# Performance work log

Hardware: AMD Instinct MI355X
Metric: run time of the kernel (lower is better)

The kernel has to match this reference:

```python
import jax, jax.numpy as jnp
import numpy as np

B, S, D = 32, 8192, 128
SPARSITY = 0.5
CLUSTER = 4
HID = 256
MEM = 128
NCLS = 10
MASK_KEY = jax.random.key(1234)


def setup_inputs() -> dict:
    key = jax.random.key(0)
    ks = jax.random.split(key, 8)
    cin = CLUSTER * D  # 512
    return {
        "x": jax.random.normal(ks[0], (B, S, D), dtype=jnp.float32),
        "memory": jax.random.normal(ks[1], (B, MEM), dtype=jnp.float32),
        "W_fc": jax.random.normal(ks[2], (HID, cin), dtype=jnp.float32) / np.sqrt(cin),
        "b_fc": jax.random.normal(ks[3], (HID,), dtype=jnp.float32) * 0.01,
        "W_mem": jax.random.normal(ks[4], (MEM, HID), dtype=jnp.float32) / np.sqrt(HID),
        "b_mem": jax.random.normal(ks[5], (MEM,), dtype=jnp.float32) * 0.01,
        "W_out": jax.random.normal(ks[6], (NCLS, MEM), dtype=jnp.float32) / np.sqrt(MEM),
        "b_out": jax.random.normal(ks[7], (NCLS,), dtype=jnp.float32) * 0.01,
    }


def reference(x, memory, W_fc, b_fc, W_mem, b_mem, W_out, b_out):
    # --- SparseInformationExtraction: top-k tokens by L2 norm ---
    k = int(SPARSITY * S)  # 4096
    token_norms = jnp.linalg.norm(x, axis=-1)          # (B, S)
    _, topk_idx = jax.lax.top_k(token_norms, k)        # (B, k), sorted desc like torch.topk
    sparse_x = jnp.take_along_axis(x, topk_idx[:, :, None], axis=1)  # (B, k, D)

    # --- HierarchicalClustering: group CLUSTER tokens ---
    num_clusters = k // CLUSTER                        # 1024
    clustered = sparse_x.reshape(B, num_clusters, CLUSTER * D)  # (B, 1024, 512)

    # --- DynamicMaskingActivation: linear + bernoulli mask + relu ---
    h = jnp.einsum('bnc,hc->bnh', clustered, W_fc) + b_fc       # (B, 1024, HID)
    mask = jax.random.bernoulli(MASK_KEY, p=SPARSITY, shape=h.shape).astype(h.dtype)
    h = jax.nn.relu(h * mask)

    # --- SparseMemory: mean-pool + linear + residual relu ---
    x_compressed = jnp.mean(h, axis=1)                           # (B, HID)
    updated_memory = jax.nn.relu(x_compressed @ W_mem.T + b_mem + memory)  # (B, MEM)

    # --- output head ---
    output = updated_memory @ W_out.T + b_out                    # (B, NCLS)
    return (output, updated_memory)
```

## Files before the change

kernel.cpp:

```cpp
#include <hip/hip_runtime.h>
#include <stdint.h>

#define NB 32
#define NS 8192
#define ND 128
#define KTOP 4096
#define NCLUST 1024
#define CIN 512
#define HIDN 256
#define NMEM 128
#define NCLS 10
#define HALFCNT 4194304u

typedef unsigned long long ull;
typedef __attribute__((ext_vector_type(8))) short bf16x8;
typedef __attribute__((ext_vector_type(4))) float f32x4;

__device__ __forceinline__ unsigned int rotl32(unsigned int v, int r) {
  return (v << r) | (v >> (32 - r));
}

__device__ __forceinline__ void threefry_block(unsigned int& x0, unsigned int& x1) {
  const unsigned int k0 = 0u;
  const unsigned int k1 = 1234u;
  const unsigned int k2 = 0x1BD11BDAu ^ 0u ^ 1234u;
  x0 += k0; x1 += k1;
#define TF_R(r) { x0 += x1; x1 = rotl32(x1, (r)); x1 ^= x0; }
  TF_R(13) TF_R(15) TF_R(26) TF_R(6)   x0 += k1; x1 += k2 + 1u;
  TF_R(17) TF_R(29) TF_R(16) TF_R(24)  x0 += k2; x1 += k0 + 2u;
  TF_R(13) TF_R(15) TF_R(26) TF_R(6)   x0 += k0; x1 += k1 + 3u;
  TF_R(17) TF_R(29) TF_R(16) TF_R(24)  x0 += k1; x1 += k2 + 4u;
  TF_R(13) TF_R(15) TF_R(26) TF_R(6)   x0 += k2; x1 += k0 + 5u;
#undef TF_R
}

__device__ __forceinline__ unsigned int f2bf(float f) {
  unsigned int u = __float_as_uint(f);
  return (u + 0x7fffu + ((u >> 16) & 1u)) >> 16;
}
__device__ __forceinline__ unsigned int pack2bf(float lo, float hi) {
  return f2bf(lo) | (f2bf(hi) << 16);
}

__device__ __forceinline__ void gload_lds16(const void* g, void* l) {
  __builtin_amdgcn_global_load_lds(
      (const __attribute__((address_space(1))) unsigned int*)g,
      (__attribute__((address_space(3))) unsigned int*)l, 16, 0, 0);
}

__device__ __forceinline__ ull shfl_xor_u64(ull x, int m) {
  unsigned int lo = (unsigned int)x, hi = (unsigned int)(x >> 32);
  lo = (unsigned int)__shfl_xor((int)lo, m);
  hi = (unsigned int)__shfl_xor((int)hi, m);
  return ((ull)hi << 32) | lo;
}

#define NORM_BLOCKS 32768
__global__ __launch_bounds__(256) void norms_kernel(
    const float* __restrict__ x, ull* __restrict__ keys,
    float* __restrict__ xc, const float* __restrict__ Wfc,
    unsigned short* __restrict__ Wbf) {
  const int blk = blockIdx.x;
  if (blk >= NORM_BLOCKS) {
    const int t = (blk - NORM_BLOCKS) * 256 + threadIdx.x;
    const float4* s = (const float4*)(Wfc + (size_t)t * 8);
    const float4 a = s[0], b = s[1];
    uint4 o;
    o.x = pack2bf(a.x, a.y); o.y = pack2bf(a.z, a.w);
    o.z = pack2bf(b.x, b.y); o.w = pack2bf(b.z, b.w);
    *(uint4*)(Wbf + (size_t)t * 8) = o;
    return;
  }
  const int t = blk * 256 + threadIdx.x;
  if (t < NB * HIDN) xc[t] = 0.0f;
  const int token = t >> 5;
  const int l = t & 31;
  const float4 v = ((const float4*)(x + (size_t)token * ND))[l];
  float ss = v.x * v.x + v.y * v.y + v.z * v.z + v.w * v.w;
#pragma unroll
  for (int off = 16; off >= 1; off >>= 1) ss += __shfl_xor(ss, off);
  if (l == 0) {
    const float nrm = sqrtf(ss);
    const unsigned int ub = ~__float_as_uint(nrm);
    keys[token] = ((ull)ub << 32) | (unsigned int)(token & (NS - 1));
  }
}

#define CMPEX(J, K, HF)                                                 \
  {                                                                     \
    _Pragma("unroll") for (int r = 0; r < 8; ++r) {                     \
      if ((r & (J)) == 0) {                                             \
        const int i0 = (tid << 3) + r;                                  \
        const bool up2 = (((i0 & (K)) == 0) != (HF));                   \
        const ull lo = v[r], hi = v[r | (J)];                           \
        const ull mn = lo < hi ? lo : hi;                               \
        const ull mx = lo < hi ? hi : lo;                               \
        v[r] = up2 ? mn : mx;                                           \
        v[r | (J)] = up2 ? mx : mn;                                     \
      }                                                                 \
    }                                                                   \
  }

__global__ __launch_bounds__(512) void sortA_kernel(ull* __restrict__ keys) {
  __shared__ ull slds[8 * 512];
  const int b = blockIdx.x >> 1;
  const int half = blockIdx.x & 1;
  const bool hf = (half != 0);
  const int tid = threadIdx.x;
  ull v[8];
  ull* base = keys + (size_t)b * NS + half * 4096;
#pragma unroll
  for (int r = 0; r < 8; ++r) v[r] = base[tid * 8 + r];

  for (int k = 2; k <= 4096; k <<= 1) {
    for (int j = k >> 1; j >= 512; j >>= 1) {
      __syncthreads();
#pragma unroll
      for (int r = 0; r < 8; ++r) slds[r * 512 + tid] = v[r];
      __syncthreads();
      const int ptid = tid ^ (j >> 3);
      const bool up2 = ((((tid << 3) & k) == 0) != hf);
      const bool lower = (((tid << 3) & j) == 0);
      const bool keepmin = (up2 == lower);
#pragma unroll
      for (int r = 0; r < 8; ++r) {
        const ull p = slds[r * 512 + ptid];
        const ull mn = v[r] < p ? v[r] : p;
        const ull mx = v[r] < p ? p : v[r];
        v[r] = keepmin ? mn : mx;
      }
    }
    {
      const int jstart = (k >> 1) < 256 ? (k >> 1) : 256;
      for (int j = jstart; j >= 8; j >>= 1) {
        const int lanemask = j >> 3;
        const bool up2 = ((((tid << 3) & k) == 0) != hf);
        const bool lower = (((tid << 3) & j) == 0);
        const bool keepmin = (up2 == lower);
#pragma unroll
        for (int r = 0; r < 8; ++r) {
          const ull p = shfl_xor_u64(v[r], lanemask);
          const ull mn = v[r] < p ? v[r] : p;
          const ull mx = v[r] < p ? p : v[r];
          v[r] = keepmin ? mn : mx;
        }
      }
    }
    if (k >= 8)      { CMPEX(4, k, hf) CMPEX(2, k, hf) CMPEX(1, k, hf) }
    else if (k == 4) { CMPEX(2, k, hf) CMPEX(1, k, hf) }
    else             { CMPEX(1, k, hf) }
  }

#pragma unroll
  for (int r = 0; r < 8; ++r) base[tid * 8 + r] = v[r];
}

__global__ __launch_bounds__(512) void sortB_kernel(
    const ull* __restrict__ keys, unsigned int* __restrict__ topk) {
  __shared__ ull slds[8 * 512];
  const int b = blockIdx.x;
  const int tid = threadIdx.x;
  ull v[8];
  const ull* base = keys + (size_t)b * NS;
#pragma unroll
  for (int r = 0; r < 8; ++r) v[r] = base[tid * 8 + r];
#pragma unroll
  for (int r = 0; r < 8; ++r) {
    const ull u = base[4096 + tid * 8 + r];
    v[r] = v[r] < u ? v[r] : u;
  }
  for (int j = 2048; j >= 512; j >>= 1) {
    __syncthreads();
#pragma unroll
    for (int r = 0; r < 8; ++r) slds[r * 512 + tid] = v[r];
    __syncthreads();
    const int ptid = tid ^ (j >> 3);
    const bool keepmin = (((tid << 3) & j) == 0);
#pragma unroll
    for (int r = 0; r < 8; ++r) {
      const ull p = slds[r * 512 + ptid];
      const ull mn = v[r] < p ? v[r] : p;
      const ull mx = v[r] < p ? p : v[r];
      v[r] = keepmin ? mn : mx;
    }
  }
  for (int j = 256; j >= 8; j >>= 1) {
    const int lanemask = j >> 3;
    const bool keepmin = (((tid << 3) & j) == 0);
#pragma unroll
    for (int r = 0; r < 8; ++r) {
      const ull p = shfl_xor_u64(v[r], lanemask);
      const ull mn = v[r] < p ? v[r] : p;
      const ull mx = v[r] < p ? p : v[r];
      v[r] = keepmin ? mn : mx;
    }
  }
  CMPEX(4, 8192, false) CMPEX(2, 8192, false) CMPEX(1, 8192, false)
#pragma unroll
  for (int r = 0; r < 8; ++r)
    topk[b * KTOP + tid * 8 + r] = (unsigned int)v[r];
}

__global__ __launch_bounds__(256, 4) void gemm_kernel(
    const float* __restrict__ x, const unsigned short* __restrict__ Wbf,
    const float* __restrict__ bfc, const unsigned int* __restrict__ topk,
    float* __restrict__ xc) {
  __shared__ __align__(16) unsigned short Al[32 * 64];
  __shared__ __align__(16) unsigned short Bl[256 * 64];
  __shared__ int tokL[128];

  const int bid = blockIdx.x;
  const int bb = bid >> 6;
  const int m0c = (bid & 63) * 16;
  const int t = threadIdx.x;
  const int w = t >> 6, l = t & 63;
  const int lrow = l & 15, lk = l >> 4;

  if (t < 128) {
    const int r = t >> 2, s = t & 3;
    const int batch = (r < 16) ? bb : bb + 16;
    tokL[t] = (int)topk[batch * KTOP + (m0c + (r & 15)) * 4 + s];
  }
  __syncthreads();

  f32x4 acc[2][4];
#pragma unroll
  for (int m = 0; m < 2; ++m)
#pragma unroll
    for (int n = 0; n < 4; ++n) acc[m][n] = (f32x4)0.f;

  const int arow = t >> 3, kq = t & 7;
  const int abatch = (arow < 16) ? bb : bb + 16;
  float4 ar[2];
  {
    const int cs = kq;
    const int token = tokL[arow * 4 + (cs >> 4)];
    const float* asrc =
        x + ((size_t)abatch * NS + token) * ND + (cs & 15) * 8;
    ar[0] = ((const float4*)asrc)[0];
    ar[1] = ((const float4*)asrc)[1];
  }

  const int brow_in8 = l >> 3;
  const int bkb_src = ((l & 7) * 16) ^ (brow_in8 << 4);

  for (int kt = 0; kt < 8; ++kt) {
    {
      uint4 p0;
      p0.x = pack2bf(ar[0].x, ar[0].y); p0.y = pack2bf(ar[0].z, ar[0].w);
      p0.z = pack2bf(ar[1].x, ar[1].y); p0.w = pack2bf(ar[1].z, ar[1].w);
      const int swz = (arow & 7) << 4;
      *(uint4*)((char*)Al + arow * 128 + ((kq * 16) ^ swz)) = p0;
    }
    {
#pragma unroll
      for (int q = 0; q < 8; ++q) {
        const int grp = w * 8 + q;
        const int row = grp * 8 + brow_in8;
        const char* g = (const char*)Wbf + (size_t)row * 1024 + kt * 128 +
                        bkb_src;
        gload_lds16(g, (char*)Bl + grp * 1024);
      }
    }
    __syncthreads();

    if (kt < 7) {
      const int cs = (kt + 1) * 8 + kq;
      const int token = tokL[arow * 4 + (cs >> 4)];
      const float* asrc =
          x + ((size_t)abatch * NS + token) * ND + (cs & 15) * 8;
      ar[0] = ((const float4*)asrc)[0];
      ar[1] = ((const float4*)asrc)[1];
    }

    const int swz = (lrow & 7) << 4;
#pragma unroll
    for (int kk = 0; kk < 2; ++kk) {
      const int koff = (kk * 64 + lk * 16) ^ swz;
      bf16x8 af[2], bfr[4];
#pragma unroll
      for (int m = 0; m < 2; ++m)
        af[m] = *(const bf16x8*)((const char*)Al +
                                 (m * 16 + lrow) * 128 + koff);
#pragma unroll
      for (int n = 0; n < 4; ++n)
        bfr[n] = *(const bf16x8*)((const char*)Bl +
                                  (w * 64 + n * 16 + lrow) * 128 + koff);
#pragma unroll
      for (int m = 0; m < 2; ++m)
#pragma unroll
        for (int n = 0; n < 4; ++n)
          acc[m][n] = __builtin_amdgcn_mfma_f32_16x16x32_bf16(
              af[m], bfr[n], acc[m][n], 0, 0, 0);
    }
    __syncthreads();
  }

  float bias_n[4];
#pragma unroll
  for (int n = 0; n < 4; ++n) bias_n[n] = bfc[w * 64 + n * 16 + lrow];

  float csum[2][4] = {{0.f, 0.f, 0.f, 0.f}, {0.f, 0.f, 0.f, 0.f}};
#pragma unroll
  for (int n = 0; n < 4; ++n) {
    const unsigned int gcol = (unsigned int)(w * 64 + n * 16 + lrow);
#pragma unroll
    for (int reg = 0; reg < 4; ++reg) {
      const unsigned int crow = (unsigned int)(m0c + lk * 4 + reg);
      const unsigned int flat = ((unsigned int)bb * 1024u + crow) * 256u + gcol;
      unsigned int a = flat, b2 = flat + HALFCNT;
      threefry_block(a, b2);
      const bool keep0 = (a & 0x80000000u) == 0u;
      const bool keep1 = (b2 & 0x80000000u) == 0u;
      float v0 = acc[0][n][reg] + bias_n[n];
      float v1 = acc[1][n][reg] + bias_n[n];
      v0 = keep0 ? fmaxf(v0, 0.0f) : 0.0f;
      v1 = keep1 ? fmaxf(v1, 0.0f) : 0.0f;
      csum[0][n] += v0;
      csum[1][n] += v1;
    }
  }
#pragma unroll
  for (int p = 0; p < 2; ++p)
#pragma unroll
    for (int n = 0; n < 4; ++n) {
      csum[p][n] += __shfl_xor(csum[p][n], 16);
      csum[p][n] += __shfl_xor(csum[p][n], 32);
    }
  if (l < 16) {
#pragma unroll
    for (int n = 0; n < 4; ++n) {
      atomicAdd(&xc[bb * HIDN + w * 64 + n * 16 + l], csum[0][n]);
      atomicAdd(&xc[(bb + 16) * HIDN + w * 64 + n * 16 + l], csum[1][n]);
    }
  }
}

__global__ __launch_bounds__(128) void tail_kernel(
    const float* __restrict__ xc, const float* __restrict__ memory,
    const float* __restrict__ Wmem, const float* __restrict__ bmem,
    const float* __restrict__ Wout, const float* __restrict__ bout,
    float* __restrict__ out) {
  __shared__ __align__(16) float xl[HIDN];
  __shared__ float ul[NMEM];
  const int b = blockIdx.x, t = threadIdx.x;
  xl[t]       = xc[b * HIDN + t] * (1.0f / NCLUST);
  xl[t + 128] = xc[b * HIDN + t + 128] * (1.0f / NCLUST);
  __syncthreads();
  float a = 0.0f;
  const float4* wr2 = (const float4*)(Wmem + (size_t)t * HIDN);
#pragma unroll 4
  for (int q = 0; q < HIDN / 4; ++q) {
    const float4 wv = wr2[q];
    const float4 xv = *(const float4*)&xl[q * 4];
    a = fmaf(wv.x, xv.x, a); a = fmaf(wv.y, xv.y, a);
    a = fmaf(wv.z, xv.z, a); a = fmaf(wv.w, xv.w, a);
  }
  a += bmem[t] + memory[b * NMEM + t];
  a = fmaxf(a, 0.0f);
  ul[t] = a;
  out[NB * NCLS + b * NMEM + t] = a;
  __syncthreads();
  if (t < NCLS) {
    float o = 0.0f;
#pragma unroll 4
    for (int m = 0; m < NMEM; ++m) o = fmaf(ul[m], Wout[t * NMEM + m], o);
    out[b * NCLS + t] = o + bout[t];
  }
}

extern "C" void kernel_launch(void* const* d_in, const int* in_sizes, int n_in,
                              void* d_out, int out_size, void* d_ws, size_t ws_size,
                              hipStream_t stream) {
  (void)in_sizes; (void)n_in; (void)out_size; (void)ws_size;
  const float* x    = (const float*)d_in[0];
  const float* mem  = (const float*)d_in[1];
  const float* Wfc  = (const float*)d_in[2];
  const float* bfc  = (const float*)d_in[3];
  const float* Wmem = (const float*)d_in[4];
  const float* bmem = (const float*)d_in[5];
  const float* Wout = (const float*)d_in[6];
  const float* bout = (const float*)d_in[7];
  float* out = (float*)d_out;

  char* ws = (char*)d_ws;
  ull* keys = (ull*)ws;
  unsigned int* topk = (unsigned int*)(ws + (size_t)NB * NS * 8);
  float* xc = (float*)(ws + (size_t)NB * NS * 8 + (size_t)NB * KTOP * 4);
  unsigned short* Wbf = (unsigned short*)(ws + (size_t)NB * NS * 8 +
                                          (size_t)NB * KTOP * 4 +
                                          (size_t)NB * HIDN * 4);

  norms_kernel<<<dim3(NORM_BLOCKS + 64), 256, 0, stream>>>(x, keys, xc, Wfc,
                                                           Wbf);
  sortA_kernel<<<dim3(NB * 2), 512, 0, stream>>>(keys);
  sortB_kernel<<<dim3(NB), 512, 0, stream>>>(keys, topk);
  gemm_kernel<<<dim3(1024), 256, 0, stream>>>(x, Wbf, bfc, topk, xc);
  tail_kernel<<<dim3(NB), 128, 0, stream>>>(xc, mem, Wmem, bmem, Wout, bout, out);
}
```

Baseline: 269.8 us.

## Precompute dropout mask bits in norms kernel and prefetch all A rows upfront

The Threefry Bernoulli mask is now generated once per element in extra blocks of the norms kernel and packed into 64-bit ballot words. The GEMM epilogue reads those bit words instead of running Threefry per accumulator element. The GEMM block mapping changes from pairing batches b and b+16 to 32 consecutive clusters of a single batch. All eight K-tiles of gathered x rows are also loaded into registers before the main loop, which raises register pressure and adds mask write/read traffic.

```diff
diff --git a/kernel.cpp b/kernel.cpp
--- a/kernel.cpp
+++ b/kernel.cpp
@@ -56,11 +56,28 @@
 }
 
 #define NORM_BLOCKS 32768
+#define WPREP_BLOCKS 64
+#define MASK_BLOCKS 16384
 __global__ __launch_bounds__(256) void norms_kernel(
     const float* __restrict__ x, ull* __restrict__ keys,
     float* __restrict__ xc, const float* __restrict__ Wfc,
-    unsigned short* __restrict__ Wbf) {
+    unsigned short* __restrict__ Wbf, ull* __restrict__ maskw) {
   const int blk = blockIdx.x;
+  if (blk >= NORM_BLOCKS + WPREP_BLOCKS) {
+    const int blkm = blk - (NORM_BLOCKS + WPREP_BLOCKS);
+    const int wv = threadIdx.x >> 6, lane = threadIdx.x & 63;
+    const unsigned int W = (unsigned int)(blkm * 4 + wv);
+    unsigned int a = W * 64u + (unsigned int)lane;
+    unsigned int b2 = a + HALFCNT;
+    threefry_block(a, b2);
+    const ull m0 = __ballot((a & 0x80000000u) == 0u);
+    const ull m1 = __ballot((b2 & 0x80000000u) == 0u);
+    if (lane == 0) {
+      maskw[W] = m0;
+      maskw[W + 65536u] = m1;
+    }
+    return;
+  }
   if (blk >= NORM_BLOCKS) {
     const int t = (blk - NORM_BLOCKS) * 256 + threadIdx.x;
     const float4* s = (const float4*)(Wfc + (size_t)t * 8);
@@ -204,51 +221,51 @@
 __global__ __launch_bounds__(256, 4) void gemm_kernel(
     const float* __restrict__ x, const unsigned short* __restrict__ Wbf,
     const float* __restrict__ bfc, const unsigned int* __restrict__ topk,
-    float* __restrict__ xc) {
+    const ull* __restrict__ maskw, float* __restrict__ xc) {
   __shared__ __align__(16) unsigned short Al[32 * 64];
   __shared__ __align__(16) unsigned short Bl[256 * 64];
   __shared__ int tokL[128];
 
   const int bid = blockIdx.x;
-  const int bb = bid >> 6;
-  const int m0c = (bid & 63) * 16;
+  const int bb = bid >> 5;
+  const int m0c = (bid & 31) * 32;
   const int t = threadIdx.x;
   const int w = t >> 6, l = t & 63;
   const int lrow = l & 15, lk = l >> 4;
 
-  if (t < 128) {
-    const int r = t >> 2, s = t & 3;
-    const int batch = (r < 16) ? bb : bb + 16;
-    tokL[t] = (int)topk[batch * KTOP + (m0c + (r & 15)) * 4 + s];
-  }
+  if (t < 128)
+    tokL[t] = (int)topk[bb * KTOP + (m0c + (t >> 2)) * 4 + (t & 3)];
   __syncthreads();
 
+  const int arow = t >> 3, kq = t & 7;
+  float4 ar[16];
+  {
+    const float* xb = x + (size_t)bb * NS * ND;
+#pragma unroll
+    for (int kt = 0; kt < 8; ++kt) {
+      const int cs = kt * 8 + kq;
+      const int token = tokL[arow * 4 + (cs >> 4)];
+      const float* asrc = xb + (size_t)token * ND + (cs & 15) * 8;
+      ar[kt * 2]     = ((const float4*)asrc)[0];
+      ar[kt * 2 + 1] = ((const float4*)asrc)[1];
+    }
+  }
+
   f32x4 acc[2][4];
 #pragma unroll
   for (int m = 0; m < 2; ++m)
 #pragma unroll
     for (int n = 0; n < 4; ++n) acc[m][n] = (f32x4)0.f;
-
-  const int arow = t >> 3, kq = t & 7;
-  const int abatch = (arow < 16) ? bb : bb + 16;
-  float4 ar[2];
-  {
-    const int cs = kq;
-    const int token = tokL[arow * 4 + (cs >> 4)];
-    const float* asrc =
-        x + ((size_t)abatch * NS + token) * ND + (cs & 15) * 8;
-    ar[0] = ((const float4*)asrc)[0];
-    ar[1] = ((const float4*)asrc)[1];
-  }
 
   const int brow_in8 = l >> 3;
   const int bkb_src = ((l & 7) * 16) ^ (brow_in8 << 4);
 
   for (int kt = 0; kt < 8; ++kt) {
     {
+      const float4 a0 = ar[kt * 2], a1 = ar[kt * 2 + 1];
       uint4 p0;
-      p0.x = pack2bf(ar[0].x, ar[0].y); p0.y = pack2bf(ar[0].z, ar[0].w);
-      p0.z = pack2bf(ar[1].x, ar[1].y); p0.w = pack2bf(ar[1].z, ar[1].w);
+      p0.x = pack2bf(a0.x, a0.y); p0.y = pack2bf(a0.z, a0.w);
+      p0.z = pack2bf(a1.x, a1.y); p0.w = pack2bf(a1.z, a1.w);
       const int swz = (arow & 7) << 4;
       *(uint4*)((char*)Al + arow * 128 + ((kq * 16) ^ swz)) = p0;
     }
@@ -264,15 +281,6 @@
     }
     __syncthreads();
 
-    if (kt < 7) {
-      const int cs = (kt + 1) * 8 + kq;
-      const int token = tokL[arow * 4 + (cs >> 4)];
-      const float* asrc =
-          x + ((size_t)abatch * NS + token) * ND + (cs & 15) * 8;
-      ar[0] = ((const float4*)asrc)[0];
-      ar[1] = ((const float4*)asrc)[1];
-    }
-
     const int swz = (lrow & 7) << 4;
 #pragma unroll
     for (int kk = 0; kk < 2; ++kk) {
@@ -300,39 +308,39 @@
 #pragma unroll
   for (int n = 0; n < 4; ++n) bias_n[n] = bfc[w * 64 + n * 16 + lrow];
 
-  float csum[2][4] = {{0.f, 0.f, 0.f, 0.f}, {0.f, 0.f, 0.f, 0.f}};
+  ull mw[2][4];
+#pragma unroll
+  for (int m = 0; m < 2; ++m)
+#pragma unroll
+    for (int reg = 0; reg < 4; ++reg) {
+      const int row = m0c + m * 16 + lk * 4 + reg;
+      mw[m][reg] = maskw[(size_t)(bb * NCLUST + row) * 4 + w];
+    }
+
+  float csum[4] = {0.f, 0.f, 0.f, 0.f};
 #pragma unroll
   for (int n = 0; n < 4; ++n) {
-    const unsigned int gcol = (unsigned int)(w * 64 + n * 16 + lrow);
-#pragma unroll
-    for (int reg = 0; reg < 4; ++reg) {
-      const unsigned int crow = (unsigned int)(m0c + lk * 4 + reg);
-      const unsigned int flat = ((unsigned int)bb * 1024u + crow) * 256u + gcol;
-      unsigned int a = flat, b2 = flat + HALFCNT;
-      threefry_block(a, b2);
-      const bool keep0 = (a & 0x80000000u) == 0u;
-      const bool keep1 = (b2 & 0x80000000u) == 0u;
-      float v0 = acc[0][n][reg] + bias_n[n];
-      float v1 = acc[1][n][reg] + bias_n[n];
-      v0 = keep0 ? fmaxf(v0, 0.0f) : 0.0f;
-      v1 = keep1 ? fmaxf(v1, 0.0f) : 0.0f;
-      csum[0][n] += v0;
-      csum[1][n] += v1;
-    }
-  }
-#pragma unroll
-  for (int p = 0; p < 2; ++p)
-#pragma unroll
-    for (int n = 0; n < 4; ++n) {
-      csum[p][n] += __shfl_xor(csum[p][n], 16);
-      csum[p][n] += __shfl_xor(csum[p][n], 32);
-    }
+    const int bit = n * 16 + lrow;
+#pragma unroll
+    for (int m = 0; m < 2; ++m) {
+#pragma unroll
+      for (int reg = 0; reg < 4; ++reg) {
+        const bool keep = ((mw[m][reg] >> bit) & 1ull) != 0ull;
+        float vv = acc[m][n][reg] + bias_n[n];
+        vv = keep ? fmaxf(vv, 0.0f) : 0.0f;
+        csum[n] += vv;
+      }
+    }
+  }
+#pragma unroll
+  for (int n = 0; n < 4; ++n) {
+    csum[n] += __shfl_xor(csum[n], 16);
+    csum[n] += __shfl_xor(csum[n], 32);
+  }
   if (l < 16) {
 #pragma unroll
-    for (int n = 0; n < 4; ++n) {
-      atomicAdd(&xc[bb * HIDN + w * 64 + n * 16 + l], csum[0][n]);
-      atomicAdd(&xc[(bb + 16) * HIDN + w * 64 + n * 16 + l], csum[1][n]);
-    }
+    for (int n = 0; n < 4; ++n)
+      atomicAdd(&xc[bb * HIDN + w * 64 + n * 16 + l], csum[n]);
   }
 }
 
@@ -384,17 +392,17 @@
   float* out = (float*)d_out;
 
   char* ws = (char*)d_ws;
-  ull* keys = (ull*)ws;
-  unsigned int* topk = (unsigned int*)(ws + (size_t)NB * NS * 8);
-  float* xc = (float*)(ws + (size_t)NB * NS * 8 + (size_t)NB * KTOP * 4);
-  unsigned short* Wbf = (unsigned short*)(ws + (size_t)NB * NS * 8 +
-                                          (size_t)NB * KTOP * 4 +
-                                          (size_t)NB * HIDN * 4);
-
-  norms_kernel<<<dim3(NORM_BLOCKS + 64), 256, 0, stream>>>(x, keys, xc, Wfc,
-                                                           Wbf);
+  size_t off = 0;
+  ull* keys = (ull*)(ws + off);          off += (size_t)NB * NS * 8;
+  unsigned int* topk = (unsigned int*)(ws + off); off += (size_t)NB * KTOP * 4;
+  float* xc = (float*)(ws + off);        off += (size_t)NB * HIDN * 4;
+  unsigned short* Wbf = (unsigned short*)(ws + off); off += (size_t)HIDN * CIN * 2;
+  ull* maskw = (ull*)(ws + off);
+
+  norms_kernel<<<dim3(NORM_BLOCKS + WPREP_BLOCKS + MASK_BLOCKS), 256, 0,
+                 stream>>>(x, keys, xc, Wfc, Wbf, maskw);
   sortA_kernel<<<dim3(NB * 2), 512, 0, stream>>>(keys);
   sortB_kernel<<<dim3(NB), 512, 0, stream>>>(keys, topk);
-  gemm_kernel<<<dim3(1024), 256, 0, stream>>>(x, Wbf, bfc, topk, xc);
+  gemm_kernel<<<dim3(1024), 256, 0, stream>>>(x, Wbf, bfc, topk, maskw, xc);
   tail_kernel<<<dim3(NB), 128, 0, stream>>>(xc, mem, Wmem, bmem, Wout, bout, out);
 }
```

Result: slower. 276.8 us (+2.6%).
